# Kernel optimization log

Hardware: AMD Instinct MI355X
Metric: run time of the kernel (lower is better)

Reference implementation:

```python
import jax, jax.numpy as jnp
import numpy as np

B, S, HID = 4, 1024, 1024
NH, HD = 16, 64  # num heads, head dim


def setup_inputs() -> dict:
    key = jax.random.key(0)
    ks = jax.random.split(key, 8)
    scale = 0.02
    return {
        "hidden_states": jax.random.normal(ks[0], (B, S, HID), dtype=jnp.float32),
        "attention_mask": jnp.ones((B, 1, 1, S), dtype=jnp.float32),
        "Wq": jax.random.normal(ks[1], (HID, HID), dtype=jnp.float32) * scale,
        "bq": jnp.zeros((HID,), dtype=jnp.float32),
        "Wk": jax.random.normal(ks[2], (HID, HID), dtype=jnp.float32) * scale,
        "bk": jnp.zeros((HID,), dtype=jnp.float32),
        "Wv": jax.random.normal(ks[3], (HID, HID), dtype=jnp.float32) * scale,
        "bv": jnp.zeros((HID,), dtype=jnp.float32),
    }


def reference(hidden_states, attention_mask, Wq, bq, Wk, bk, Wv, bv):
    # Linear projections: torch nn.Linear computes x @ W.T + b
    q = hidden_states @ Wq.T + bq  # [B,S,HID]
    k = hidden_states @ Wk.T + bk
    v = hidden_states @ Wv.T + bv

    def split_heads(x):
        return x.reshape(B, S, NH, HD).transpose(0, 2, 1, 3)  # [B,NH,S,HD]

    q, k, v = split_heads(q), split_heads(k), split_heads(v)

    scores = jnp.einsum("bhqd,bhkd->bhqk", q, k) / jnp.sqrt(jnp.float32(HD))
    # faithful to original: scores - (2 - mask) * 1e6
    scores = scores - (2.0 - attention_mask) * 1.0e6
    probs = jax.nn.softmax(scores, axis=-1)
    # dropout: eval mode -> identity
    ctx = jnp.einsum("bhqk,bhkd->bhqd", probs, v)  # [B,NH,S,HD]
    ctx = ctx.transpose(0, 2, 1, 3).reshape(B, S, HID)
    return ctx
```

## Files before the change

### kernel.cpp

```cpp
#include <hip/hip_runtime.h>
#include <math.h>

#define B_ 4
#define S_ 1024
#define HID_ 1024
#define NH_ 16
#define HD_ 64
#define NTOK (B_ * S_)

typedef __attribute__((ext_vector_type(4))) float f32x4;
typedef __attribute__((ext_vector_type(16))) float f32x16;
typedef __attribute__((ext_vector_type(8))) short bf16x8;

__device__ __forceinline__ unsigned short f2bf(float f) {
    union { float f; unsigned int u; } v; v.f = f;
    unsigned int r = v.u + 0x7fffu + ((v.u >> 16) & 1u);
    return (unsigned short)(r >> 16);
}

#if __has_builtin(__builtin_amdgcn_cvt_pk_bf16_f32)
__device__ __forceinline__ unsigned int pk_bf16(float a, float b) {
    auto v = __builtin_amdgcn_cvt_pk_bf16_f32(a, b);
    union { decltype(v) v; unsigned int u; } cv; cv.v = v;
    return cv.u;
}
#else
__device__ __forceinline__ unsigned int pk_bf16(float a, float b) {
    return (unsigned int)f2bf(a) | ((unsigned int)f2bf(b) << 16);
}
#endif

#if __has_builtin(__builtin_amdgcn_permlane32_swap)
__device__ __forceinline__ void plswap(unsigned &a, unsigned &b) {
    typedef __attribute__((ext_vector_type(2))) int v2i;
    v2i r = __builtin_amdgcn_permlane32_swap((int)a, (int)b, false, false);
    a = (unsigned)r[0]; b = (unsigned)r[1];
}
#else
__device__ __forceinline__ void plswap(unsigned &a, unsigned &b) {
    const unsigned bl = __shfl_xor(b, 32);
    const unsigned ah = __shfl_xor(a, 32);
    const bool hi = ((threadIdx.x & 63) >> 5) != 0;
    const unsigned na = hi ? bl : a;
    const unsigned nb = hi ? b  : ah;
    a = na; b = nb;
}
#endif

__device__ __forceinline__ void load_lds16(const void* g, void* l) {
    __builtin_amdgcn_global_load_lds(
        (const __attribute__((address_space(1))) unsigned int*)(uintptr_t)g,
        (__attribute__((address_space(3))) unsigned int*)(uintptr_t)l,
        16, 0, 0);
}

__global__ __launch_bounds__(256) void cvt_all(
    const float* __restrict__ x, const float* __restrict__ wq,
    const float* __restrict__ wk, const float* __restrict__ wv,
    unsigned short* __restrict__ xb, unsigned short* __restrict__ wqb,
    unsigned short* __restrict__ wkb, unsigned short* __restrict__ wvb)
{
    const int which = blockIdx.y;
    const float* src = which == 0 ? x : which == 1 ? wq : which == 2 ? wk : wv;
    unsigned short* dst = which == 0 ? xb : which == 1 ? wqb : which == 2 ? wkb : wvb;
    const int n4 = (which == 0) ? (NTOK * HID_ / 4) : (HID_ * HID_ / 4);
    int i = blockIdx.x * 256 + threadIdx.x;
    if (i < n4) {
        float4 f = ((const float4*)src)[i];
        uint2 o;
        o.x = pk_bf16(f.x, f.y);
        o.y = pk_bf16(f.z, f.w);
        ((uint2*)dst)[i] = o;
    }
}

__global__ __launch_bounds__(512, 2) void qkv_gemm_mfma(
    const unsigned short* __restrict__ xb,
    const unsigned short* __restrict__ Wqb, const float* __restrict__ bq,
    const unsigned short* __restrict__ Wkb, const float* __restrict__ bk,
    const unsigned short* __restrict__ Wvb, const float* __restrict__ bv,
    unsigned short* __restrict__ qout, unsigned short* __restrict__ kout,
    unsigned short* __restrict__ vtout)
{
    extern __shared__ char sm[];

    const int which = blockIdx.z;
    const unsigned short* __restrict__ W = which == 0 ? Wqb : which == 1 ? Wkb : Wvb;
    const float* __restrict__ bias       = which == 0 ? bq  : which == 1 ? bk  : bv;

    const int t    = threadIdx.x;
    const int lane = t & 63;
    const int w    = t >> 6;
    const int wr   = w >> 2;
    const int wc   = w & 3;
    const int g    = lane >> 4;
    const int lrow = lane & 15;

    const unsigned short* __restrict__ Arow = (which == 2) ? W  : xb;
    const unsigned short* __restrict__ Brow = (which == 2) ? xb : W;
    const int am0 = (which == 2) ? blockIdx.y * 256 : blockIdx.x * 256;
    const int bn0 = (which == 2) ? blockIdx.x * 256 : blockIdx.y * 256;

    const int r0  = t >> 2;
    const int c0  = t & 3;
    const int csw = (c0 ^ ((r0 >> 1) & 3)) << 3;
    const unsigned short* gA = Arow + (size_t)(am0 + r0) * HID_ + csw;
    const unsigned short* gB = Brow + (size_t)(bn0 + r0) * HID_ + csw;

    const int sw4  = (g ^ ((lrow >> 1) & 3)) << 4;
    const int aoff = wr * 8192 + lrow * 64 + sw4;
    const int boff = wc * 4096 + lrow * 64 + sw4;

    f32x4 acc[8][4];
    #pragma unroll
    for (int m = 0; m < 8; ++m)
        #pragma unroll
        for (int n = 0; n < 4; ++n) acc[m][n] = (f32x4){0.f, 0.f, 0.f, 0.f};

    auto stageA = [&](int nb, int ks, int kt1) {
        char* dst = sm + ((nb * 2 + ks) << 14);
        const unsigned short* s = gA + kt1 * 64 + ks * 32;
        load_lds16(s, dst + t * 16);
        load_lds16(s + (size_t)128 * HID_, dst + (t + 512) * 16);
    };
    auto stageB = [&](int nb, int ks, int kt1) {
        char* dst = sm + 65536 + ((nb * 2 + ks) << 14);
        const unsigned short* s = gB + kt1 * 64 + ks * 32;
        load_lds16(s, dst + t * 16);
        load_lds16(s + (size_t)128 * HID_, dst + (t + 512) * 16);
    };

    stageA(0, 0, 0); stageB(0, 0, 0); stageA(0, 1, 0); stageB(0, 1, 0);
    asm volatile("s_waitcnt vmcnt(4)" ::: "memory");
    __builtin_amdgcn_s_barrier();

    for (int kt = 0; kt < 16; ++kt) {
        const int cur = kt & 1, nb = cur ^ 1;
        const bool nl = (kt < 15);
        const char* A0 = sm + ((cur * 2 + 0) << 14);
        const char* A1 = sm + ((cur * 2 + 1) << 14);
        const char* B0 = sm + 65536 + ((cur * 2 + 0) << 14);
        const char* B1 = sm + 65536 + ((cur * 2 + 1) << 14);
        bf16x8 bf[4];

        {
            bf16x8 af[4];
            #pragma unroll
            for (int m = 0; m < 4; ++m) af[m] = *(const bf16x8*)(A0 + aoff + m * 1024);
            #pragma unroll
            for (int n = 0; n < 4; ++n) bf[n] = *(const bf16x8*)(B0 + boff + n * 1024);
            if (nl) stageA(nb, 0, kt + 1);
            __builtin_amdgcn_s_barrier();
            __builtin_amdgcn_s_setprio(1);
            #pragma unroll
            for (int m = 0; m < 4; ++m)
                #pragma unroll
                for (int n = 0; n < 4; ++n)
                    acc[m][n] = __builtin_amdgcn_mfma_f32_16x16x32_bf16(
                        af[m], bf[n], acc[m][n], 0, 0, 0);
            __builtin_amdgcn_s_setprio(0);
        }
        {
            bf16x8 af[4];
            #pragma unroll
            for (int m = 0; m < 4; ++m) af[m] = *(const bf16x8*)(A0 + aoff + (4 + m) * 1024);
            if (nl) {
                stageB(nb, 0, kt + 1);
                asm volatile("s_waitcnt vmcnt(4)" ::: "memory");
            } else {
                asm volatile("s_waitcnt vmcnt(0)" ::: "memory");
            }
            __builtin_amdgcn_s_barrier();
            __builtin_amdgcn_s_setprio(1);
            #pragma unroll
            for (int m = 0; m < 4; ++m)
                #pragma unroll
                for (int n = 0; n < 4; ++n)
                    acc[4 + m][n] = __builtin_amdgcn_mfma_f32_16x16x32_bf16(
                        af[m], bf[n], acc[4 + m][n], 0, 0, 0);
            __builtin_amdgcn_s_setprio(0);
        }
        {
            bf16x8 af[4];
            #pragma unroll
            for (int m = 0; m < 4; ++m) af[m] = *(const bf16x8*)(A1 + aoff + m * 1024);
            #pragma unroll
            for (int n = 0; n < 4; ++n) bf[n] = *(const bf16x8*)(B1 + boff + n * 1024);
            if (nl) stageA(nb, 1, kt + 1);
            __builtin_amdgcn_s_barrier();
            __builtin_amdgcn_s_setprio(1);
            #pragma unroll
            for (int m = 0; m < 4; ++m)
                #pragma unroll
                for (int n = 0; n < 4; ++n)
                    acc[m][n] = __builtin_amdgcn_mfma_f32_16x16x32_bf16(
                        af[m], bf[n], acc[m][n], 0, 0, 0);
            __builtin_amdgcn_s_setprio(0);
        }
        {
            bf16x8 af[4];
            #pragma unroll
            for (int m = 0; m < 4; ++m) af[m] = *(const bf16x8*)(A1 + aoff + (4 + m) * 1024);
            if (nl) {
                stageB(nb, 1, kt + 1);
                asm volatile("s_waitcnt vmcnt(4)" ::: "memory");
            }
            __builtin_amdgcn_s_barrier();
            __builtin_amdgcn_s_setprio(1);
            #pragma unroll
            for (int m = 0; m < 4; ++m)
                #pragma unroll
                for (int n = 0; n < 4; ++n)
                    acc[4 + m][n] = __builtin_amdgcn_mfma_f32_16x16x32_bf16(
                        af[m], bf[n], acc[4 + m][n], 0, 0, 0);
            __builtin_amdgcn_s_setprio(0);
        }
    }

    const int col   = lane & 15;
    const int rbase = (lane >> 4) << 2;
    if (which == 2) {
        #pragma unroll
        for (int m = 0; m < 8; ++m) {
            #pragma unroll
            for (int rr = 0; rr < 4; ++rr) {
                const int feat = am0 + wr * 128 + m * 16 + rbase + rr;
                const int h = feat >> 6, d = feat & 63;
                const float bias_v = bias[feat];
                #pragma unroll
                for (int n = 0; n < 4; ++n) {
                    const int tok = bn0 + wc * 64 + n * 16 + col;
                    const int b = tok >> 10, s = tok & 1023;
                    vtout[((size_t)((b << 4) + h) << 16) + ((size_t)d << 10) + s] =
                        f2bf(acc[m][n][rr] + bias_v);
                }
            }
        }
    } else {
        #pragma unroll
        for (int n = 0; n < 4; ++n) {
            const int feat = bn0 + wc * 64 + n * 16 + col;
            const int h = feat >> 6, d = feat & 63;
            const float bias_v = bias[feat];
            #pragma unroll
            for (int m = 0; m < 8; ++m) {
                #pragma unroll
                for (int rr = 0; rr < 4; ++rr) {
                    const int tok = am0 + wr * 128 + m * 16 + rbase + rr;
                    const int b = tok >> 10, s = tok & 1023;
                    const size_t off = ((size_t)((b << 4) + h) << 16) + ((size_t)s << 6) + d;
                    const float val = acc[m][n][rr] + bias_v;
                    if (which == 0) qout[off] = f2bf(val);
                    else            kout[off] = f2bf(val);
                }
            }
        }
    }
}

__global__ __launch_bounds__(512, 4) void attn_mfma(
    const unsigned short* __restrict__ Q, const unsigned short* __restrict__ K,
    const unsigned short* __restrict__ Vt, const float* __restrict__ mask,
    float* __restrict__ out)
{
    __shared__ unsigned short Ks[2][2][64 * 64];
    __shared__ unsigned short Vts[2][64 * 64];
    __shared__ float Mts[1024];

    const int t    = threadIdx.x;
    const int lane = t & 63;
    const int w    = t >> 6;
    const int kh   = w >> 2;
    const int pw   = w & 3;
    const int q31  = lane & 31;
    const int hl   = lane >> 5;

    const int bh = blockIdx.x;
    const int b  = bh >> 4;
    const int h  = bh & 15;
    const int q0w = (blockIdx.y << 7) + (pw << 5);

    const unsigned short* __restrict__ qg = Q  + ((size_t)bh << 16);
    const unsigned short* __restrict__ kg = K  + ((size_t)bh << 16);
    const unsigned short* __restrict__ vg = Vt + ((size_t)bh << 16);

    bf16x8 qreg[4];
    {
        const unsigned short* qp = qg + ((size_t)(q0w + q31) << 6);
        #pragma unroll
        for (int kc = 0; kc < 4; ++kc)
            qreg[kc] = *(const bf16x8*)&qp[kc * 16 + (hl << 3)];
    }

    int fro[4];
    #pragma unroll
    for (int kc = 0; kc < 4; ++kc)
        fro[kc] = q31 * 128 + ((((kc << 1) + hl) ^ (q31 & 7)) << 4);

    const int srow = t >> 3;
    const int c8   = ((t & 7) ^ (srow & 7)) << 3;
    const unsigned short* kstat = kg + (size_t)srow * 64 + c8;
    const unsigned short* vstat = vg + (size_t)srow * 1024 + c8;

    f32x16 O[2];
    #pragma unroll
    for (int i = 0; i < 16; ++i) { O[0][i] = 0.f; O[1][i] = 0.f; }
    float lacc = 0.f;

    #pragma unroll
    for (int hh = 0; hh < 2; ++hh)
        load_lds16(kstat + hh * 32768, (char*)Ks[hh][0] + t * 16);
    #pragma unroll
    for (int i = 0; i < 2; ++i) {
        const int key = t + i * 512;
        Mts[key] = (2.0f - mask[(b << 10) + key]) * 1.0e6f;
    }
    __syncthreads();

    for (int kt = 0; kt < 8; ++kt) {
        const int cur = kt & 1;

        #pragma unroll
        for (int hh = 0; hh < 2; ++hh) {
            load_lds16(vstat + hh * 512 + (size_t)kt * 64, (char*)Vts[hh] + t * 16);
            if (kt < 7)
                load_lds16(kstat + hh * 32768 + (size_t)(kt + 1) * 4096,
                           (char*)Ks[hh][cur ^ 1] + t * 16);
        }

        const char* Kb = (const char*)Ks[kh][cur];
        const char* Vb = (const char*)Vts[kh];

        f32x16 sacc[2];
        #pragma unroll
        for (int i = 0; i < 16; ++i) { sacc[0][i] = 0.f; sacc[1][i] = 0.f; }
        #pragma unroll
        for (int kb = 0; kb < 2; ++kb) {
            bf16x8 kf[4];
            #pragma unroll
            for (int kc = 0; kc < 4; ++kc)
                kf[kc] = *(const bf16x8*)(Kb + kb * 4096 + fro[kc]);
            __builtin_amdgcn_s_setprio(1);
            #pragma unroll
            for (int kc = 0; kc < 4; ++kc)
                sacc[kb] = __builtin_amdgcn_mfma_f32_32x32x16_bf16(
                    kf[kc], qreg[kc], sacc[kb], 0, 0, 0);
            __builtin_amdgcn_s_setprio(0);
        }

        bf16x8 pf[4];
        #pragma unroll
        for (int kb = 0; kb < 2; ++kb) {
            unsigned u[4][2];
            #pragma unroll
            for (int rq = 0; rq < 4; ++rq) {
                const f32x4 m4 = *(const f32x4*)&Mts[(kh << 9) + kt * 64 + kb * 32 + rq * 8 + (hl << 2)];
                float p[4];
                #pragma unroll
                for (int r = 0; r < 4; ++r) {
                    const float sv = sacc[kb][rq * 4 + r] * 0.125f - m4[r];
                    p[r] = __expf(sv + 1.0e6f);
                }
                lacc += (p[0] + p[1]) + (p[2] + p[3]);
                u[rq][0] = pk_bf16(p[0], p[1]);
                u[rq][1] = pk_bf16(p[2], p[3]);
            }
            #pragma unroll
            for (int c = 0; c < 2; ++c) {
                unsigned w0 = u[2 * c][0], w2 = u[2 * c + 1][0];
                plswap(w0, w2);
                unsigned w1 = u[2 * c][1], w3 = u[2 * c + 1][1];
                plswap(w1, w3);
                union { unsigned uu[4]; bf16x8 v; } f;
                f.uu[0] = w0; f.uu[1] = w1; f.uu[2] = w2; f.uu[3] = w3;
                pf[kb * 2 + c] = f.v;
            }
        }

        __syncthreads();

        #pragma unroll
        for (int hb = 0; hb < 2; ++hb) {
            bf16x8 vf[4];
            #pragma unroll
            for (int kc = 0; kc < 4; ++kc)
                vf[kc] = *(const bf16x8*)(Vb + hb * 4096 + fro[kc]);
            __builtin_amdgcn_s_setprio(1);
            #pragma unroll
            for (int kc = 0; kc < 4; ++kc)
                O[hb] = __builtin_amdgcn_mfma_f32_32x32x16_bf16(
                    pf[kc], vf[kc], O[hb], 0, 0, 0);
            __builtin_amdgcn_s_setprio(0);
        }

        __syncthreads();
    }

    float* Osh = (float*)&Ks[0][0][0];
    float* Lsh = (float*)&Vts[0][0];
    const float l = lacc + __shfl_xor(lacc, 32);
    if (kh == 1) {
        #pragma unroll
        for (int r = 0; r < 16; ++r) {
            const int qr = (r & 3) + ((r >> 2) << 3) + (hl << 2);
            Osh[pw * 2048 + qr * 64 + q31]      = O[0][r];
            Osh[pw * 2048 + qr * 64 + 32 + q31] = O[1][r];
        }
        if (lane < 32) Lsh[pw * 32 + q31] = l;
    } else {
        if (lane < 32) Lsh[128 + pw * 32 + q31] = l;
    }
    __syncthreads();
    if (kh == 0) {
        #pragma unroll
        for (int r = 0; r < 16; ++r) {
            const int qr = (r & 3) + ((r >> 2) << 3) + (hl << 2);
            const float inv = 1.0f / (Lsh[128 + pw * 32 + qr] + Lsh[pw * 32 + qr]);
            const size_t base = (((size_t)(b << 10) + (q0w + qr)) << 10) + (h << 6);
            out[base + q31]      = (O[0][r] + Osh[pw * 2048 + qr * 64 + q31])      * inv;
            out[base + 32 + q31] = (O[1][r] + Osh[pw * 2048 + qr * 64 + 32 + q31]) * inv;
        }
    }
}

extern "C" void kernel_launch(void* const* d_in, const int* in_sizes, int n_in,
                              void* d_out, int out_size, void* d_ws, size_t ws_size,
                              hipStream_t stream) {
    const float* hs   = (const float*)d_in[0];
    const float* mask = (const float*)d_in[1];
    const float* Wq   = (const float*)d_in[2];
    const float* bq   = (const float*)d_in[3];
    const float* Wk   = (const float*)d_in[4];
    const float* bk   = (const float*)d_in[5];
    const float* Wv   = (const float*)d_in[6];
    const float* bv   = (const float*)d_in[7];
    float* out = (float*)d_out;

    char* ws = (char*)d_ws;
    unsigned short* xb  = (unsigned short*)(ws);
    unsigned short* wqb = (unsigned short*)(ws + ((size_t)8  << 20));
    unsigned short* wkb = (unsigned short*)(ws + ((size_t)10 << 20));
    unsigned short* wvb = (unsigned short*)(ws + ((size_t)12 << 20));
    unsigned short* qb  = (unsigned short*)(ws + ((size_t)14 << 20));
    unsigned short* kb  = (unsigned short*)(ws + ((size_t)22 << 20));
    unsigned short* vtb = (unsigned short*)(ws + ((size_t)30 << 20));

    static bool attr_set = false;
    if (!attr_set) {
        hipFuncSetAttribute((const void*)qkv_gemm_mfma,
                            hipFuncAttributeMaxDynamicSharedMemorySize, 131072);
        attr_set = true;
    }

    cvt_all<<<dim3(4096, 4), 256, 0, stream>>>(hs, Wq, Wk, Wv, xb, wqb, wkb, wvb);
    qkv_gemm_mfma<<<dim3(NTOK / 256, HID_ / 256, 3), 512, 131072, stream>>>(
        xb, wqb, bq, wkb, bk, wvb, bv, qb, kb, vtb);
    attn_mfma<<<dim3(B_ * NH_, S_ / 128), 512, 0, stream>>>(qb, kb, vtb, mask, out);
}
```

Measured before the change: 147.7 us.

## Restructure projection GEMM into four-stage LDS ring with three-tile prefetch

Replaces the double-buffered 64-wide K pipeline in the QKV projection GEMM with a four-slot ring of 32-wide K tiles. Global-to-LDS loads now run three tiles ahead. The barrier comes before the next stage is issued, and vmcnt waits are tuned per iteration. The goal is to hide more global-load latency behind MFMA work, at the cost of more loop iterations and barriers per K step.

```diff
diff --git a/kernel.cpp b/kernel.cpp
--- a/kernel.cpp
+++ b/kernel.cpp
@@ -117,40 +117,36 @@
         #pragma unroll
         for (int n = 0; n < 4; ++n) acc[m][n] = (f32x4){0.f, 0.f, 0.f, 0.f};
 
-    auto stageA = [&](int nb, int ks, int kt1) {
-        char* dst = sm + ((nb * 2 + ks) << 14);
-        const unsigned short* s = gA + kt1 * 64 + ks * 32;
+    auto stageA = [&](int kt) {
+        char* dst = sm + (kt & 3) * 32768;
+        const unsigned short* s = gA + kt * 32;
         load_lds16(s, dst + t * 16);
-        load_lds16(s + (size_t)128 * HID_, dst + (t + 512) * 16);
+        load_lds16(s + (size_t)128 * HID_, dst + 8192 + t * 16);
     };
-    auto stageB = [&](int nb, int ks, int kt1) {
-        char* dst = sm + 65536 + ((nb * 2 + ks) << 14);
-        const unsigned short* s = gB + kt1 * 64 + ks * 32;
+    auto stageB = [&](int kt) {
+        char* dst = sm + (kt & 3) * 32768 + 16384;
+        const unsigned short* s = gB + kt * 32;
         load_lds16(s, dst + t * 16);
-        load_lds16(s + (size_t)128 * HID_, dst + (t + 512) * 16);
+        load_lds16(s + (size_t)128 * HID_, dst + 8192 + t * 16);
     };
 
-    stageA(0, 0, 0); stageB(0, 0, 0); stageA(0, 1, 0); stageB(0, 1, 0);
-    asm volatile("s_waitcnt vmcnt(4)" ::: "memory");
-    __builtin_amdgcn_s_barrier();
-
-    for (int kt = 0; kt < 16; ++kt) {
-        const int cur = kt & 1, nb = cur ^ 1;
-        const bool nl = (kt < 15);
-        const char* A0 = sm + ((cur * 2 + 0) << 14);
-        const char* A1 = sm + ((cur * 2 + 1) << 14);
-        const char* B0 = sm + 65536 + ((cur * 2 + 0) << 14);
-        const char* B1 = sm + 65536 + ((cur * 2 + 1) << 14);
+    stageA(0); stageB(0); stageA(1); stageB(1); stageA(2); stageB(2);
+    asm volatile("s_waitcnt vmcnt(8)" ::: "memory");
+    asm volatile("s_barrier" ::: "memory");
+
+    for (int kt = 0; kt < 32; ++kt) {
+        const char* Ab = sm + (kt & 3) * 32768;
+        const char* Bb = Ab + 16384;
         bf16x8 bf[4];
 
         {
             bf16x8 af[4];
             #pragma unroll
-            for (int m = 0; m < 4; ++m) af[m] = *(const bf16x8*)(A0 + aoff + m * 1024);
-            #pragma unroll
-            for (int n = 0; n < 4; ++n) bf[n] = *(const bf16x8*)(B0 + boff + n * 1024);
-            if (nl) stageA(nb, 0, kt + 1);
-            __builtin_amdgcn_s_barrier();
+            for (int m = 0; m < 4; ++m) af[m] = *(const bf16x8*)(Ab + aoff + m * 1024);
+            #pragma unroll
+            for (int n = 0; n < 4; ++n) bf[n] = *(const bf16x8*)(Bb + boff + n * 1024);
+            asm volatile("s_barrier" ::: "memory");
+            if (kt < 29) stageA(kt + 3);
             __builtin_amdgcn_s_setprio(1);
             #pragma unroll
             for (int m = 0; m < 4; ++m)
@@ -163,49 +159,16 @@
         {
             bf16x8 af[4];
             #pragma unroll
-            for (int m = 0; m < 4; ++m) af[m] = *(const bf16x8*)(A0 + aoff + (4 + m) * 1024);
-            if (nl) {
-                stageB(nb, 0, kt + 1);
+            for (int m = 0; m < 4; ++m) af[m] = *(const bf16x8*)(Ab + aoff + (4 + m) * 1024);
+            if (kt < 29) stageB(kt + 3);
+            if (kt <= 28) {
+                asm volatile("s_waitcnt vmcnt(8)" ::: "memory");
+            } else if (kt == 29) {
                 asm volatile("s_waitcnt vmcnt(4)" ::: "memory");
-            } else {
+            } else if (kt == 30) {
                 asm volatile("s_waitcnt vmcnt(0)" ::: "memory");
             }
-            __builtin_amdgcn_s_barrier();
-            __builtin_amdgcn_s_setprio(1);
-            #pragma unroll
-            for (int m = 0; m < 4; ++m)
-                #pragma unroll
-                for (int n = 0; n < 4; ++n)
-                    acc[4 + m][n] = __builtin_amdgcn_mfma_f32_16x16x32_bf16(
-                        af[m], bf[n], acc[4 + m][n], 0, 0, 0);
-            __builtin_amdgcn_s_setprio(0);
-        }
-        {
-            bf16x8 af[4];
-            #pragma unroll
-            for (int m = 0; m < 4; ++m) af[m] = *(const bf16x8*)(A1 + aoff + m * 1024);
-            #pragma unroll
-            for (int n = 0; n < 4; ++n) bf[n] = *(const bf16x8*)(B1 + boff + n * 1024);
-            if (nl) stageA(nb, 1, kt + 1);
-            __builtin_amdgcn_s_barrier();
-            __builtin_amdgcn_s_setprio(1);
-            #pragma unroll
-            for (int m = 0; m < 4; ++m)
-                #pragma unroll
-                for (int n = 0; n < 4; ++n)
-                    acc[m][n] = __builtin_amdgcn_mfma_f32_16x16x32_bf16(
-                        af[m], bf[n], acc[m][n], 0, 0, 0);
-            __builtin_amdgcn_s_setprio(0);
-        }
-        {
-            bf16x8 af[4];
-            #pragma unroll
-            for (int m = 0; m < 4; ++m) af[m] = *(const bf16x8*)(A1 + aoff + (4 + m) * 1024);
-            if (nl) {
-                stageB(nb, 1, kt + 1);
-                asm volatile("s_waitcnt vmcnt(4)" ::: "memory");
-            }
-            __builtin_amdgcn_s_barrier();
+            asm volatile("s_barrier" ::: "memory");
             __builtin_amdgcn_s_setprio(1);
             #pragma unroll
             for (int m = 0; m < 4; ++m)
```

Measured after the change: 150.1 us. About the same (+1.6%).
